# Optimization experiments

Hardware: AMD Instinct MI355X
Metric: run time of the kernel (lower is better)

## Reference

```python
import jax, jax.numpy as jnp
import numpy as np

DIM = 4096
BATCH = 64
DEFAULT_LR = 0.001
DEFAULT_ALPHA = 0.01
EPS = 1e-08


def setup_inputs() -> dict:
    key = jax.random.key(0)
    k1, k2, k3 = jax.random.split(key, 3)
    weight = jax.random.normal(k1, (DIM, DIM), dtype=jnp.float32)
    input_x = jax.random.normal(k2, (BATCH, DIM), dtype=jnp.float32)
    grad = jax.random.normal(k3, (DIM, DIM), dtype=jnp.float32)
    return {"weight": weight, "input_x": input_x, "grad": grad}


def reference(weight, input_x, grad):
    # L2-normalize inputs along last dim (normalize_inputs=True)
    x = input_x / (jnp.linalg.norm(input_x, axis=-1, keepdims=True) + EPS)
    # batched outer product averaged over batch: (dim, dim)
    outer = jnp.einsum('bi,bj->ij', x, x) / x.shape[0]
    decay_matrix = jnp.eye(DIM, dtype=weight.dtype) - DEFAULT_ALPHA * outer
    # W_{t+1} = W @ (I - alpha * outer) - lr * grad
    new_weight = weight @ decay_matrix - DEFAULT_LR * grad
    return new_weight
```

## Files before the change

kernel.cpp:

```cpp
#include <hip/hip_runtime.h>
#include <math.h>

#define DIM 4096
#define BATCH 64

typedef __attribute__((ext_vector_type(8))) short short8;
typedef __attribute__((ext_vector_type(4))) float f32x4;
typedef __attribute__((ext_vector_type(4))) unsigned int u32x4;

__device__ __forceinline__ float4 ld4(const float* p) {
    return *reinterpret_cast<const float4*>(p);
}

__device__ __forceinline__ unsigned short f2bf(float f) {
    unsigned u = __builtin_bit_cast(unsigned, f);
    u = (u + 0x7fffu + ((u >> 16) & 1u)) >> 16;
    return (unsigned short)u;
}

__device__ __forceinline__ unsigned pack_bf2(float x, float y) {
    return (__builtin_bit_cast(unsigned, x) >> 16) |
           (__builtin_bit_cast(unsigned, y) & 0xffff0000u);
}

__global__ __launch_bounds__(256) void k_norm(const float* __restrict__ x,
                                              unsigned short* __restrict__ xb1,
                                              unsigned short* __restrict__ xb2) {
    const int b = blockIdx.x;
    const int tid = threadIdx.x;
    const float* row = x + (size_t)b * DIM;

    float ss = 0.f;
    for (int k = tid * 4; k < DIM; k += 256 * 4) {
        float4 v = ld4(row + k);
        ss += v.x * v.x + v.y * v.y + v.z * v.z + v.w * v.w;
    }
#pragma unroll
    for (int m = 32; m >= 1; m >>= 1) ss += __shfl_xor(ss, m, 64);

    __shared__ float wsum[4];
    if ((tid & 63) == 0) wsum[tid >> 6] = ss;
    __syncthreads();
    const float total = wsum[0] + wsum[1] + wsum[2] + wsum[3];
    const float scale = 1.0f / (sqrtf(total) + 1e-8f);

    const int bt = b >> 4;
    const int li = b & 15;
    const int ks = b >> 5;
    const int hi = (b & 31) >> 3;
    const int jr = b & 7;

    for (int k = tid; k < DIM; k += 256) {
        const float v = row[k] * scale;
        const unsigned short h = f2bf(v);
        const int l1 = li | (((k & 31) >> 3) << 4);
        xb1[(size_t)((((bt * 128) + (k >> 5)) * 64 + l1) << 3) + (k & 7)] = h;
        const int l2 = (k & 15) | (hi << 4);
        xb2[(size_t)(((((k >> 4) * 2) + ks) * 64 + l2) << 3) + jr] = h;
    }
}

__global__ __launch_bounds__(1024, 8) void k_fused(const float* __restrict__ W,
                                                   const float* __restrict__ G,
                                                   const unsigned short* __restrict__ xb1,
                                                   const unsigned short* __restrict__ xb2,
                                                   float* __restrict__ out) {
    __shared__ __align__(16) float lds[17472];
    float* yp = lds;
    float* y2 = lds + 16384;

    const int tid = threadIdx.x;
    const int wv = tid >> 6;
    const int l  = tid & 63;
    const int lr = l & 15;
    const int lh = l >> 4;

    const int bid = blockIdx.x;
    const int sid = (bid & 7) * 64 + (bid >> 3);
    const int rt  = sid >> 1;
    const int half = sid & 1;
    const int i0 = rt * 16;

    f32x4 acc0 = {0.f, 0.f, 0.f, 0.f};
    f32x4 acc1 = acc0, acc2 = acc0, acc3 = acc0;
    const short8* xb1v = (const short8*)xb1;

#pragma unroll 2
    for (int s = 0; s < 8; ++s) {
        const int kbg = wv * 8 + s;
        const float* wp = W + (size_t)(i0 + lr) * DIM + kbg * 32 + lh * 8;
        const float4 wa = ld4(wp);
        const float4 wb = ld4(wp + 4);
        const int bs = kbg * 64 + l;
        const short8 b0 = xb1v[bs];
        const short8 b1 = xb1v[bs + 8192];
        const short8 b2 = xb1v[bs + 16384];
        const short8 b3 = xb1v[bs + 24576];
        u32x4 ap;
        ap[0] = pack_bf2(wa.x, wa.y);
        ap[1] = pack_bf2(wa.z, wa.w);
        ap[2] = pack_bf2(wb.x, wb.y);
        ap[3] = pack_bf2(wb.z, wb.w);
        const short8 a = __builtin_bit_cast(short8, ap);
        acc0 = __builtin_amdgcn_mfma_f32_16x16x32_bf16(a, b0, acc0, 0, 0, 0);
        acc1 = __builtin_amdgcn_mfma_f32_16x16x32_bf16(a, b1, acc1, 0, 0, 0);
        acc2 = __builtin_amdgcn_mfma_f32_16x16x32_bf16(a, b2, acc2, 0, 0, 0);
        acc3 = __builtin_amdgcn_mfma_f32_16x16x32_bf16(a, b3, acc3, 0, 0, 0);
    }
    {
        f32x4* dst = (f32x4*)yp;
        dst[(wv * 4 + 0) * 64 + l] = acc0;
        dst[(wv * 4 + 1) * 64 + l] = acc1;
        dst[(wv * 4 + 2) * 64 + l] = acc2;
        dst[(wv * 4 + 3) * 64 + l] = acc3;
    }
    __syncthreads();

    {
        const int r  = tid >> 6;
        const int bb = tid & 63;
        const int btt = bb >> 4;
        const int lii = (bb & 15) | ((r >> 2) << 4);
        const int jq  = r & 3;
        float s = 0.f;
#pragma unroll
        for (int w = 0; w < 16; ++w) s += yp[(((w * 4 + btt) * 64 + lii) << 2) + jq];
        y2[r * 68 + bb] = s;
    }
    __syncthreads();

    const float NC = -0.01f / 64.0f;
    short8 ya0, ya1;
#pragma unroll
    for (int j = 0; j < 8; ++j) {
        ya0[j] = (short)f2bf(NC * y2[lr * 68 + lh * 8 + j]);
        ya1[j] = (short)f2bf(NC * y2[lr * 68 + 32 + lh * 8 + j]);
    }
    __syncthreads();

    constexpr float LRc = 0.001f;
    const short8* xb2v = (const short8*)xb2;
    float* dl = lds + wv * 1088;
    const int colbase = half * 2048 + wv * 128;
    const int cc4 = (l & 15) * 4;
    const int rr0 = l >> 4;

    for (int c = 0; c < 2; ++c) {
        const int col0 = colbase + c * 64;
        const int jt0 = col0 >> 4;
        f32x4 dt[4];
#pragma unroll
        for (int tl = 0; tl < 4; ++tl) {
            const int bslot = (jt0 + tl) * 128 + l;
            f32x4 d = {0.f, 0.f, 0.f, 0.f};
            d = __builtin_amdgcn_mfma_f32_16x16x32_bf16(ya0, xb2v[bslot], d, 0, 0, 0);
            d = __builtin_amdgcn_mfma_f32_16x16x32_bf16(ya1, xb2v[bslot + 64], d, 0, 0, 0);
            dt[tl] = d;
        }
#pragma unroll
        for (int tl = 0; tl < 4; ++tl)
#pragma unroll
            for (int q = 0; q < 4; ++q)
                dl[(lh * 4 + q) * 68 + tl * 16 + lr] = dt[tl][q];

        float4 w4[4], g4[4];
#pragma unroll
        for (int i = 0; i < 4; ++i) {
            const size_t gidx = (size_t)(i0 + rr0 + 4 * i) * DIM + col0 + cc4;
            w4[i] = ld4(W + gidx);
            g4[i] = ld4(G + gidx);
        }
#pragma unroll
        for (int i = 0; i < 4; ++i) {
            const float4 dd = ld4(dl + (rr0 + 4 * i) * 68 + cc4);
            const size_t gidx = (size_t)(i0 + rr0 + 4 * i) * DIM + col0 + cc4;
            float4 o;
            o.x = w4[i].x - LRc * g4[i].x + dd.x;
            o.y = w4[i].y - LRc * g4[i].y + dd.y;
            o.z = w4[i].z - LRc * g4[i].z + dd.z;
            o.w = w4[i].w - LRc * g4[i].w + dd.w;
            *reinterpret_cast<float4*>(out + gidx) = o;
        }
    }
}

extern "C" void kernel_launch(void* const* d_in, const int* in_sizes, int n_in,
                              void* d_out, int out_size, void* d_ws, size_t ws_size,
                              hipStream_t stream) {
    const float* W = (const float*)d_in[0];
    const float* X = (const float*)d_in[1];
    const float* G = (const float*)d_in[2];
    float* out = (float*)d_out;

    unsigned short* xb1 = (unsigned short*)d_ws;
    unsigned short* xb2 = xb1 + (size_t)DIM * BATCH;

    hipLaunchKernelGGL(k_norm, dim3(BATCH), dim3(256), 0, stream, X, xb1, xb2);
    hipLaunchKernelGGL(k_fused, dim3(512), dim3(1024), 0, stream,
                       W, G, xb1, xb2, out);
}
```

Baseline: 65.48 us.

## Process full row tile per block instead of splitting columns across two blocks

Each block now owns a 16-row tile across all 4096 columns, so grid is 256 blocks instead of 512. The per-row y projection (W@x) is no longer computed redundantly by two blocks. The epilogue handles wider 128-column chunks with larger LDS staging, and G loads and output stores become nontemporal. The cost is a larger LDS footprint and fewer blocks, which lowers occupancy. The XCD-aware block index remapping is also dropped.

```diff
diff --git a/kernel.cpp b/kernel.cpp
--- a/kernel.cpp
+++ b/kernel.cpp
@@ -60,12 +60,12 @@
     }
 }
 
-__global__ __launch_bounds__(1024, 8) void k_fused(const float* __restrict__ W,
+__global__ __launch_bounds__(1024, 4) void k_fused(const float* __restrict__ W,
                                                    const float* __restrict__ G,
                                                    const unsigned short* __restrict__ xb1,
                                                    const unsigned short* __restrict__ xb2,
                                                    float* __restrict__ out) {
-    __shared__ __align__(16) float lds[17472];
+    __shared__ __align__(16) float lds[33792];
     float* yp = lds;
     float* y2 = lds + 16384;
 
@@ -74,12 +74,7 @@
     const int l  = tid & 63;
     const int lr = l & 15;
     const int lh = l >> 4;
-
-    const int bid = blockIdx.x;
-    const int sid = (bid & 7) * 64 + (bid >> 3);
-    const int rt  = sid >> 1;
-    const int half = sid & 1;
-    const int i0 = rt * 16;
+    const int i0 = blockIdx.x * 16;
 
     f32x4 acc0 = {0.f, 0.f, 0.f, 0.f};
     f32x4 acc1 = acc0, acc2 = acc0, acc3 = acc0;
@@ -140,46 +135,47 @@
 
     constexpr float LRc = 0.001f;
     const short8* xb2v = (const short8*)xb2;
-    float* dl = lds + wv * 1088;
-    const int colbase = half * 2048 + wv * 128;
-    const int cc4 = (l & 15) * 4;
-    const int rr0 = l >> 4;
+    float* dl = lds + wv * 2112;
+    const int c32 = (l & 31) * 4;
+    const int r0 = l >> 5;
 
     for (int c = 0; c < 2; ++c) {
-        const int col0 = colbase + c * 64;
-        const int jt0 = col0 >> 4;
-        f32x4 dt[4];
+        f32x4 dt[8];
 #pragma unroll
-        for (int tl = 0; tl < 4; ++tl) {
-            const int bslot = (jt0 + tl) * 128 + l;
+        for (int tl = 0; tl < 8; ++tl) {
+            const int jt = wv * 16 + c * 8 + tl;
+            const int bslot = jt * 128 + l;
             f32x4 d = {0.f, 0.f, 0.f, 0.f};
             d = __builtin_amdgcn_mfma_f32_16x16x32_bf16(ya0, xb2v[bslot], d, 0, 0, 0);
             d = __builtin_amdgcn_mfma_f32_16x16x32_bf16(ya1, xb2v[bslot + 64], d, 0, 0, 0);
             dt[tl] = d;
         }
 #pragma unroll
-        for (int tl = 0; tl < 4; ++tl)
+        for (int tl = 0; tl < 8; ++tl)
 #pragma unroll
             for (int q = 0; q < 4; ++q)
-                dl[(lh * 4 + q) * 68 + tl * 16 + lr] = dt[tl][q];
+                dl[(lh * 4 + q) * 132 + tl * 16 + lr] = dt[tl][q];
 
-        float4 w4[4], g4[4];
+        const int colg = wv * 256 + c * 128 + c32;
+        float4 wv4[8];
+        f32x4 gv4[8];
 #pragma unroll
-        for (int i = 0; i < 4; ++i) {
-            const size_t gidx = (size_t)(i0 + rr0 + 4 * i) * DIM + col0 + cc4;
-            w4[i] = ld4(W + gidx);
-            g4[i] = ld4(G + gidx);
+        for (int i = 0; i < 8; ++i) {
+            const size_t gidx = (size_t)(i0 + r0 + 2 * i) * DIM + colg;
+            wv4[i] = ld4(W + gidx);
+            gv4[i] = __builtin_nontemporal_load(
+                         reinterpret_cast<const f32x4*>(G + gidx));
         }
 #pragma unroll
-        for (int i = 0; i < 4; ++i) {
-            const float4 dd = ld4(dl + (rr0 + 4 * i) * 68 + cc4);
-            const size_t gidx = (size_t)(i0 + rr0 + 4 * i) * DIM + col0 + cc4;
-            float4 o;
-            o.x = w4[i].x - LRc * g4[i].x + dd.x;
-            o.y = w4[i].y - LRc * g4[i].y + dd.y;
-            o.z = w4[i].z - LRc * g4[i].z + dd.z;
-            o.w = w4[i].w - LRc * g4[i].w + dd.w;
-            *reinterpret_cast<float4*>(out + gidx) = o;
+        for (int i = 0; i < 8; ++i) {
+            const float4 dd = ld4(dl + (r0 + 2 * i) * 132 + c32);
+            const size_t gidx = (size_t)(i0 + r0 + 2 * i) * DIM + colg;
+            f32x4 o;
+            o[0] = wv4[i].x - LRc * gv4[i][0] + dd.x;
+            o[1] = wv4[i].y - LRc * gv4[i][1] + dd.y;
+            o[2] = wv4[i].z - LRc * gv4[i][2] + dd.z;
+            o[3] = wv4[i].w - LRc * gv4[i][3] + dd.w;
+            __builtin_nontemporal_store(o, reinterpret_cast<f32x4*>(out + gidx));
         }
     }
 }
@@ -196,6 +192,6 @@
     unsigned short* xb2 = xb1 + (size_t)DIM * BATCH;
 
     hipLaunchKernelGGL(k_norm, dim3(BATCH), dim3(256), 0, stream, X, xb1, xb2);
-    hipLaunchKernelGGL(k_fused, dim3(512), dim3(1024), 0, stream,
+    hipLaunchKernelGGL(k_fused, dim3(DIM / 16), dim3(1024), 0, stream,
                        W, G, xb1, xb2, out);
 }
```

After: 64.22 us. Within noise of the previous version (-1.9%).
